# Kernel tuning notes

Measured on AMD Instinct MI355X. Metric: run time of the kernel, lower is better.

Reference implementation:

```python
import jax, jax.numpy as jnp
import numpy as np

N_GROUPS = 32
EPS = 1e-5
N_HEADS = 8
D_K = 64


def setup_inputs() -> dict:
    key = jax.random.key(0)
    ks = jax.random.split(key, 4)
    B, C, H, W = 16, 512, 32, 32
    x = jax.random.normal(ks[0], (B, C, H, W), dtype=jnp.float32)
    gn_w = jnp.ones((C,), dtype=jnp.float32)
    gn_b = jnp.zeros((C,), dtype=jnp.float32)
    proj_w = jax.random.normal(ks[1], (3 * C, C), dtype=jnp.float32) * (C ** -0.5)
    proj_b = jnp.zeros((3 * C,), dtype=jnp.float32)
    out_w = jax.random.normal(ks[2], (C, C), dtype=jnp.float32) * (C ** -0.5)
    out_b = jnp.zeros((C,), dtype=jnp.float32)
    return {"x": x, "gn_w": gn_w, "gn_b": gn_b, "proj_w": proj_w,
            "proj_b": proj_b, "out_w": out_w, "out_b": out_b}


def _group_norm(x, w, b):
    B, C, H, W = x.shape
    xg = x.reshape(B, N_GROUPS, C // N_GROUPS, H, W)
    mean = xg.mean(axis=(2, 3, 4), keepdims=True)
    var = xg.var(axis=(2, 3, 4), keepdims=True)
    xn = (xg - mean) * jax.lax.rsqrt(var + EPS)
    xn = xn.reshape(B, C, H, W)
    return xn * w[None, :, None, None] + b[None, :, None, None]


def reference(x, gn_w, gn_b, proj_w, proj_b, out_w, out_b):
    B, C, H, W = x.shape
    S = H * W
    scale = D_K ** -0.25  # applied to both q and k, as in the original
    h = _group_norm(x, gn_w, gn_b).reshape(B, C, S).transpose(0, 2, 1)  # [B,S,C]
    qkv = h @ proj_w.T + proj_b  # [B,S,3C]
    qkv = qkv.reshape(B, S, N_HEADS, 3 * D_K)
    q, k, v = jnp.split(qkv, 3, axis=-1)  # each [B,S,H,D]
    attn = jnp.einsum('bihd,bjhd->bijh', q * scale, k * scale)  # [B,S,S,Hd]
    attn = jax.nn.softmax(attn, axis=2)
    res = jnp.einsum('bijh,bjhd->bihd', attn, v).reshape(B, S, N_HEADS * D_K)
    res = res @ out_w.T + out_b  # [B,S,C]
    res = res.transpose(0, 2, 1).reshape(B, C, H, W)
    return res + x
```

## Files before the change

### kernel.cpp

```cpp
#include <hip/hip_runtime.h>
#include <stdint.h>

typedef unsigned short u16;
typedef __attribute__((ext_vector_type(8))) short bf16x8;
typedef __attribute__((ext_vector_type(4))) short bf16x4;
typedef __attribute__((ext_vector_type(4))) float f32x4;
typedef __attribute__((ext_vector_type(4))) unsigned short u16x4;

#define GLD16(gp, lp) __builtin_amdgcn_global_load_lds( \
    (__attribute__((address_space(1))) void*)(void*)(gp), \
    (__attribute__((address_space(3))) void*)(void*)(lp), 16, 0, 0)

__device__ __forceinline__ u16 f2b(float f) {
  union { float f; unsigned u; } v; v.f = f;
  unsigned r = v.u + 0x7FFFu + ((v.u >> 16) & 1u);
  return (u16)(r >> 16);
}

__device__ __forceinline__ float fexp2(float x) {
#if __has_builtin(__builtin_amdgcn_exp2f)
  return __builtin_amdgcn_exp2f(x);
#else
  return exp2f(x);
#endif
}

__global__ __launch_bounds__(256) void cvt_kernel(const float* __restrict__ wq_f,
                                                  const float* __restrict__ wo_f,
                                                  u16* __restrict__ wq,
                                                  u16* __restrict__ wo) {
  int i = blockIdx.x * 256 + threadIdx.x;
  const float* src; u16* dst; int j;
  if (i < 196608) { src = wq_f; dst = wq; j = i; }
  else            { src = wo_f; dst = wo; j = i - 196608; }
  const float4 f = ((const float4*)src)[j];
  u16x4 r; r[0] = f2b(f.x); r[1] = f2b(f.y); r[2] = f2b(f.z); r[3] = f2b(f.w);
  *(u16x4*)(dst + (size_t)j * 4) = r;
}

__global__ __launch_bounds__(256) void gn_kernel(const float* __restrict__ x,
                                                 const float* __restrict__ gw,
                                                 const float* __restrict__ gb,
                                                 u16* __restrict__ h) {
  const int b = blockIdx.x >> 5, g = blockIdx.x & 31;
  const float* xg = x + ((size_t)(b * 512 + g * 16)) * 1024;
  const int tid = threadIdx.x;
  float4 vals[16];
  float s = 0.f, ss = 0.f;
#pragma unroll
  for (int j = 0; j < 16; j++) {
    const float4 v = ((const float4*)xg)[j * 256 + tid];
    vals[j] = v;
    s  += (v.x + v.y) + (v.z + v.w);
    ss += (v.x * v.x + v.y * v.y) + (v.z * v.z + v.w * v.w);
  }
#pragma unroll
  for (int off = 32; off; off >>= 1) { s += __shfl_down(s, off); ss += __shfl_down(ss, off); }
  __shared__ float red[8];
  const int wid = tid >> 6, lane = tid & 63;
  if (lane == 0) { red[wid] = s; red[4 + wid] = ss; }
  __syncthreads();
  if (tid == 0) {
    float S = red[0] + red[1] + red[2] + red[3];
    float SS = red[4] + red[5] + red[6] + red[7];
    float mean = S * (1.f / 16384.f);
    float var = SS * (1.f / 16384.f) - mean * mean;
    red[0] = mean; red[1] = rsqrtf(var + 1e-5f);
  }
  __syncthreads();
  const float mean = red[0], rs = red[1];
  float sc[16], bi[16];
#pragma unroll
  for (int c = 0; c < 16; c++) { sc[c] = gw[g * 16 + c] * rs; bi[c] = gb[g * 16 + c]; }
  u16* dst = h + ((size_t)(b * 32 + g) * 1024 + 4 * tid) * 16;
#pragma unroll
  for (int e = 0; e < 4; e++) {
    u16 row[16];
#pragma unroll
    for (int j = 0; j < 16; j++) {
      const float v = (e == 0) ? vals[j].x : (e == 1) ? vals[j].y : (e == 2) ? vals[j].z : vals[j].w;
      row[j] = f2b((v - mean) * sc[j] + bi[j]);
    }
    *(bf16x8*)(dst + e * 16) = *(bf16x8*)&row[0];
    *(bf16x8*)(dst + e * 16 + 8) = *(bf16x8*)&row[8];
  }
}

__global__ __launch_bounds__(256) void qkv_gemm(const u16* __restrict__ h,
                                                const u16* __restrict__ w,
                                                const float* __restrict__ bias,
                                                u16* __restrict__ q,
                                                u16* __restrict__ k,
                                                u16* __restrict__ v) {
  __shared__ u16 As[128 * 32];
  __shared__ u16 Bs[128 * 32];
  const int b = blockIdx.z;
  const int bm = blockIdx.x;
  const int bn = blockIdx.y;
  const int tid = threadIdx.x, lane = tid & 63, wid = tid >> 6;
  const int wm = wid & 1, wn = wid >> 1;
  const u16* gA = h + (size_t)b * 524288 + (size_t)bm * 128 * 16;
  const u16* gB = w + (size_t)bn * 128 * 512;

  const f32x4 fz = {0.f, 0.f, 0.f, 0.f};
  f32x4 acc[4][4];
#pragma unroll
  for (int i = 0; i < 4; i++)
#pragma unroll
    for (int j = 0; j < 4; j++) acc[i][j] = fz;

  const int r0 = lane >> 2;
  const int ch8 = (lane & 3) * 8;

  for (int kt = 0; kt < 16; ++kt) {
    __syncthreads();
    const int chA = kt * 32 + ch8;
    const int gstrip = chA >> 4, rem = chA & 15;
#pragma unroll
    for (int j = 0; j < 2; ++j) {
      const int idx = wid * 2 + j;
      const int row = idx * 16 + r0;
      GLD16(gA + (size_t)gstrip * 16384 + (size_t)row * 16 + rem, &As[idx * 512 + lane * 8]);
      GLD16(gB + (size_t)row * 512 + kt * 32 + ch8, &Bs[idx * 512 + lane * 8]);
    }
    __syncthreads();
    bf16x8 af[4], bf[4];
#pragma unroll
    for (int mi = 0; mi < 4; mi++)
      af[mi] = *(const bf16x8*)&As[(wm * 64 + mi * 16 + (lane & 15)) * 32 + (lane >> 4) * 8];
#pragma unroll
    for (int ni = 0; ni < 4; ni++)
      bf[ni] = *(const bf16x8*)&Bs[(wn * 64 + ni * 16 + (lane & 15)) * 32 + (lane >> 4) * 8];
#pragma unroll
    for (int mi = 0; mi < 4; mi++)
#pragma unroll
      for (int ni = 0; ni < 4; ni++)
        acc[mi][ni] = __builtin_amdgcn_mfma_f32_16x16x32_bf16(af[mi], bf[ni], acc[mi][ni], 0, 0, 0);
  }

  const float qscale = 0.51006972f;
  const float kscale = 0.35355339059327373f;
  const int quad4 = (lane >> 4) << 2;
#pragma unroll
  for (int mi = 0; mi < 4; mi++) {
    const int m = bm * 128 + wm * 64 + mi * 16 + quad4;
#pragma unroll
    for (int ni = 0; ni < 4; ni++) {
      const int n = bn * 128 + wn * 64 + ni * 16 + (lane & 15);
      const int head = n / 192;
      const int rr = n - head * 192;
      const float bi = bias[n];
      const int d = rr & 63;
      if (rr < 128) {
        u16* dst = (rr < 64) ? q : k;
        const float sc = (rr < 64) ? qscale : kscale;
        dst += ((size_t)(b * 8 + head) * 1024 + m) * 64 + d;
#pragma unroll
        for (int r = 0; r < 4; r++)
          dst[(size_t)r * 64] = f2b((acc[mi][ni][r] + bi) * sc);
      } else {
        u16x4 pk;
#pragma unroll
        for (int r = 0; r < 4; r++) pk[r] = f2b(acc[mi][ni][r] + bi);
        *(u16x4*)(v + ((size_t)(b * 8 + head) * 64 + d) * 1024 + m) = pk;
      }
    }
  }
}

__global__ __launch_bounds__(512) void attn_kernel(const u16* __restrict__ q,
                                                   const u16* __restrict__ k,
                                                   const u16* __restrict__ vT,
                                                   u16* __restrict__ o) {
  __shared__ u16 Ks[2][64 * 64];
  __shared__ u16 Vs[2][64 * 64];
  const int bh = blockIdx.x;
  const int qb = blockIdx.y;
  const int tid = threadIdx.x, lane = tid & 63, wid = tid >> 6;
  const u16* Q = q + (size_t)bh * 1024 * 64;
  const u16* K = k + (size_t)bh * 1024 * 64;
  const u16* V = vT + (size_t)bh * 64 * 1024;
  const int qrow0 = qb * 256 + wid * 32;
  const int c15 = lane & 15, quad = lane >> 4;
  const int sw = c15 & 7;
  const int srow = tid >> 3;
  const int u8g  = tid & 7;
  const int s7 = srow & 7;
  const int kld = srow * 64 + ((u8g ^ s7) * 8);
  const int ve = 4 * (u8g >> 2) + 2 * (u8g & 1);
  const int vc = ((u8g >> 1) & 1) * 4;
  const int vld0 = srow * 64 + ((ve ^ s7) * 8) + vc;
  const int vld1 = srow * 64 + (((ve + 1) ^ s7) * 8) + vc;

  bf16x8 qf[2][2];
#pragma unroll
  for (int kk = 0; kk < 2; kk++)
#pragma unroll
    for (int ni = 0; ni < 2; ni++)
      qf[kk][ni] = *(const bf16x8*)(Q + (size_t)(qrow0 + ni * 16 + c15) * 64 + kk * 32 + quad * 8);

  const f32x4 fz = {0.f, 0.f, 0.f, 0.f};
  const float Mshift = 14.4269504089f;
  const f32x4 fm = {-Mshift, -Mshift, -Mshift, -Mshift};
  f32x4 oaccT[4][2];
#pragma unroll
  for (int i = 0; i < 4; i++)
#pragma unroll
    for (int j = 0; j < 2; j++) oaccT[i][j] = fz;
  float lsum[2] = {0.f, 0.f};

  bf16x8 kr, vr;
  kr = *(const bf16x8*)(K + (size_t)srow * 64 + u8g * 8);
  vr = *(const bf16x8*)(V + (size_t)srow * 1024 + u8g * 8);
  {
    u16* Kd = Ks[0]; u16* Vd = Vs[0];
    *(bf16x8*)&Kd[kld] = kr;
    union { bf16x4 h[2]; bf16x8 v; } a; a.v = vr;
    *(bf16x4*)&Vd[vld0] = a.h[0];
    *(bf16x4*)&Vd[vld1] = a.h[1];
  }
  kr = *(const bf16x8*)(K + (size_t)(64 + srow) * 64 + u8g * 8);
  vr = *(const bf16x8*)(V + (size_t)srow * 1024 + 64 + u8g * 8);

  for (int kt = 0; kt < 16; ++kt) {
    __syncthreads();
    const int cur = kt & 1, alt = cur ^ 1;
    if (kt < 15) {
      u16* Kd = Ks[alt]; u16* Vd = Vs[alt];
      *(bf16x8*)&Kd[kld] = kr;
      union { bf16x4 h[2]; bf16x8 v; } a; a.v = vr;
      *(bf16x4*)&Vd[vld0] = a.h[0];
      *(bf16x4*)&Vd[vld1] = a.h[1];
      const int pk2 = (kt + 2) & 15;
      kr = *(const bf16x8*)(K + ((size_t)pk2 * 64 + srow) * 64 + u8g * 8);
      vr = *(const bf16x8*)(V + (size_t)srow * 1024 + pk2 * 64 + u8g * 8);
    }
    const u16* Kc = Ks[cur];
    const u16* Vc = Vs[cur];

    f32x4 sacc[4][2];
#pragma unroll
    for (int i = 0; i < 4; i++)
#pragma unroll
      for (int j = 0; j < 2; j++) sacc[i][j] = fm;
#pragma unroll
    for (int kk = 0; kk < 2; kk++) {
      bf16x8 af[4];
#pragma unroll
      for (int mi = 0; mi < 4; mi++)
        af[mi] = *(const bf16x8*)&Kc[(mi * 16 + c15) * 64 + (((kk * 4 + quad) ^ sw) * 8)];
      __builtin_amdgcn_s_setprio(1);
#pragma unroll
      for (int mi = 0; mi < 4; mi++)
#pragma unroll
        for (int ni = 0; ni < 2; ni++)
          sacc[mi][ni] = __builtin_amdgcn_mfma_f32_16x16x32_bf16(af[mi], qf[kk][ni], sacc[mi][ni], 0, 0, 0);
      __builtin_amdgcn_s_setprio(0);
    }

    unsigned pkd[4][2][2];
#pragma unroll
    for (int ni = 0; ni < 2; ni++) {
      float ls = 0.f;
#pragma unroll
      for (int mi = 0; mi < 4; mi++) {
        unsigned pu[4];
#pragma unroll
        for (int r = 0; r < 4; r++) {
          const float p = fexp2(sacc[mi][ni][r]);
          ls += p;
          union { float f; unsigned u; } c; c.f = p;
          pu[r] = c.u;
        }
        pkd[mi][ni][0] = __builtin_amdgcn_perm(pu[1], pu[0], 0x07060302u);
        pkd[mi][ni][1] = __builtin_amdgcn_perm(pu[3], pu[2], 0x07060302u);
      }
      lsum[ni] += ls;
    }

#pragma unroll
    for (int mg = 0; mg < 2; mg++) {
      union { unsigned u[4]; bf16x8 v; } bb[2];
#pragma unroll
      for (int ni = 0; ni < 2; ni++) {
        bb[ni].u[0] = pkd[2 * mg][ni][0];     bb[ni].u[1] = pkd[2 * mg][ni][1];
        bb[ni].u[2] = pkd[2 * mg + 1][ni][0]; bb[ni].u[3] = pkd[2 * mg + 1][ni][1];
      }
      bf16x8 aa[4];
#pragma unroll
      for (int nd = 0; nd < 4; nd++)
        aa[nd] = *(const bf16x8*)&Vc[(nd * 16 + c15) * 64 + (((mg * 4 + quad) ^ sw) * 8)];
      __builtin_amdgcn_s_setprio(1);
#pragma unroll
      for (int nd = 0; nd < 4; nd++)
#pragma unroll
        for (int ni = 0; ni < 2; ni++)
          oaccT[nd][ni] = __builtin_amdgcn_mfma_f32_16x16x32_bf16(aa[nd], bb[ni].v, oaccT[nd][ni], 0, 0, 0);
      __builtin_amdgcn_s_setprio(0);
    }
  }

  float iv[2];
#pragma unroll
  for (int ni = 0; ni < 2; ni++) {
    float l = lsum[ni];
    l += __shfl_xor(l, 16);
    l += __shfl_xor(l, 32);
    iv[ni] = 1.f / l;
  }
  const int b = bh >> 3, hh = bh & 7;
#pragma unroll
  for (int ni = 0; ni < 2; ni++) {
    const int row = qrow0 + ni * 16 + c15;
#pragma unroll
    for (int nd = 0; nd < 4; nd++) {
      u16x4 pk4;
#pragma unroll
      for (int r = 0; r < 4; r++) pk4[r] = f2b(oaccT[nd][ni][r] * iv[ni]);
      *(u16x4*)(o + ((size_t)b * 1024 + row) * 512 + hh * 64 + nd * 16 + quad * 4) = pk4;
    }
  }
}

__global__ __launch_bounds__(256) void out_gemm(const u16* __restrict__ attn,
                                                const u16* __restrict__ wo,
                                                const float* __restrict__ ob,
                                                const float* __restrict__ x,
                                                float* __restrict__ out) {
  __shared__ u16 As[128 * 32];
  __shared__ u16 Bs[128 * 32];
  const int b = blockIdx.z;
  const int bm = blockIdx.x;
  const int bn = blockIdx.y;
  const int tid = threadIdx.x, lane = tid & 63, wid = tid >> 6;
  const int wm = wid & 1, wn = wid >> 1;
  const u16* gA = attn + ((size_t)b * 1024 + bm * 128) * 512;
  const u16* gB = wo + (size_t)bn * 128 * 512;

  const f32x4 fz = {0.f, 0.f, 0.f, 0.f};
  f32x4 acc[4][4];
#pragma unroll
  for (int i = 0; i < 4; i++)
#pragma unroll
    for (int j = 0; j < 4; j++) acc[i][j] = fz;

  const int r0 = lane >> 2;
  const int ch8 = (lane & 3) * 8;

  for (int kt = 0; kt < 16; ++kt) {
    __syncthreads();
#pragma unroll
    for (int j = 0; j < 2; ++j) {
      const int idx = wid * 2 + j;
      const int row = idx * 16 + r0;
      GLD16(gA + (size_t)row * 512 + kt * 32 + ch8, &As[idx * 512 + lane * 8]);
      GLD16(gB + (size_t)row * 512 + kt * 32 + ch8, &Bs[idx * 512 + lane * 8]);
    }
    __syncthreads();
    bf16x8 af[4], bf[4];
#pragma unroll
    for (int mi = 0; mi < 4; mi++)
      af[mi] = *(const bf16x8*)&As[(wm * 64 + mi * 16 + (lane & 15)) * 32 + (lane >> 4) * 8];
#pragma unroll
    for (int ni = 0; ni < 4; ni++)
      bf[ni] = *(const bf16x8*)&Bs[(wn * 64 + ni * 16 + (lane & 15)) * 32 + (lane >> 4) * 8];
#pragma unroll
    for (int mi = 0; mi < 4; mi++)
#pragma unroll
      for (int ni = 0; ni < 4; ni++)
        acc[mi][ni] = __builtin_amdgcn_mfma_f32_16x16x32_bf16(af[mi], bf[ni], acc[mi][ni], 0, 0, 0);
  }

  const int quad4 = (lane >> 4) << 2;
  const int c15_ = lane & 15;
#pragma unroll
  for (int mi = 0; mi < 4; mi++) {
    const int m = bm * 128 + wm * 64 + mi * 16 + quad4;
#pragma unroll
    for (int ni = 0; ni < 4; ni++) {
      const int c = bn * 128 + wn * 64 + ni * 16 + c15_;
      const float bo = ob[c];
      const size_t idx = ((size_t)b * 512 + c) * 1024 + m;
      const float4 xv = *(const float4*)(x + idx);
      float4 ov;
      ov.x = acc[mi][ni][0] + bo + xv.x;
      ov.y = acc[mi][ni][1] + bo + xv.y;
      ov.z = acc[mi][ni][2] + bo + xv.z;
      ov.w = acc[mi][ni][3] + bo + xv.w;
      *(float4*)(out + idx) = ov;
    }
  }
}

extern "C" void kernel_launch(void* const* d_in, const int* in_sizes, int n_in,
                              void* d_out, int out_size, void* d_ws, size_t ws_size,
                              hipStream_t stream) {
  const float* x      = (const float*)d_in[0];
  const float* gn_w   = (const float*)d_in[1];
  const float* gn_b   = (const float*)d_in[2];
  const float* proj_w = (const float*)d_in[3];
  const float* proj_b = (const float*)d_in[4];
  const float* out_w  = (const float*)d_in[5];
  const float* out_b  = (const float*)d_in[6];
  float* out = (float*)d_out;

  char* p = (char*)d_ws;
  u16* h    = (u16*)p; p += (size_t)16 * 1024 * 512 * 2;
  u16* q    = (u16*)p; p += (size_t)16 * 8 * 1024 * 64 * 2;
  u16* k    = (u16*)p; p += (size_t)16 * 8 * 1024 * 64 * 2;
  u16* v    = (u16*)p; p += (size_t)16 * 8 * 1024 * 64 * 2;
  u16* attn = (u16*)p; p += (size_t)16 * 1024 * 512 * 2;
  u16* wq   = (u16*)p; p += (size_t)1536 * 512 * 2;
  u16* wo   = (u16*)p; p += (size_t)512 * 512 * 2;

  cvt_kernel<<<1024, 256, 0, stream>>>(proj_w, out_w, wq, wo);
  gn_kernel<<<512, 256, 0, stream>>>(x, gn_w, gn_b, h);
  qkv_gemm<<<dim3(8, 12, 16), 256, 0, stream>>>(h, wq, proj_b, q, k, v);
  attn_kernel<<<dim3(128, 4), 512, 0, stream>>>(q, k, v, attn);
  out_gemm<<<dim3(8, 4, 16), 256, 0, stream>>>(attn, wo, out_b, x, out);
}
```

Measured before the change: 210.4 us.

## Merge groupnorm and weight conversion; rewrite QKV GEMM with larger double-buffered tiles

```diff
diff --git a/kernel.cpp b/kernel.cpp
--- a/kernel.cpp
+++ b/kernel.cpp
@@ -25,23 +25,24 @@
 #endif
 }
 
-__global__ __launch_bounds__(256) void cvt_kernel(const float* __restrict__ wq_f,
-                                                  const float* __restrict__ wo_f,
-                                                  u16* __restrict__ wq,
-                                                  u16* __restrict__ wo) {
-  int i = blockIdx.x * 256 + threadIdx.x;
-  const float* src; u16* dst; int j;
-  if (i < 196608) { src = wq_f; dst = wq; j = i; }
-  else            { src = wo_f; dst = wo; j = i - 196608; }
-  const float4 f = ((const float4*)src)[j];
-  u16x4 r; r[0] = f2b(f.x); r[1] = f2b(f.y); r[2] = f2b(f.z); r[3] = f2b(f.w);
-  *(u16x4*)(dst + (size_t)j * 4) = r;
-}
-
-__global__ __launch_bounds__(256) void gn_kernel(const float* __restrict__ x,
-                                                 const float* __restrict__ gw,
-                                                 const float* __restrict__ gb,
-                                                 u16* __restrict__ h) {
+__global__ __launch_bounds__(256) void gncvt_kernel(const float* __restrict__ x,
+                                                    const float* __restrict__ gw,
+                                                    const float* __restrict__ gb,
+                                                    u16* __restrict__ h,
+                                                    const float* __restrict__ wq_f,
+                                                    const float* __restrict__ wo_f,
+                                                    u16* __restrict__ wq,
+                                                    u16* __restrict__ wo) {
+  if (blockIdx.x >= 512) {
+    int i = (blockIdx.x - 512) * 256 + threadIdx.x;
+    const float* src; u16* dst; int j;
+    if (i < 196608) { src = wq_f; dst = wq; j = i; }
+    else            { src = wo_f; dst = wo; j = i - 196608; }
+    const float4 f = ((const float4*)src)[j];
+    u16x4 r; r[0] = f2b(f.x); r[1] = f2b(f.y); r[2] = f2b(f.z); r[3] = f2b(f.w);
+    *(u16x4*)(dst + (size_t)j * 4) = r;
+    return;
+  }
   const int b = blockIdx.x >> 5, g = blockIdx.x & 31;
   const float* xg = x + ((size_t)(b * 512 + g * 16)) * 1024;
   const int tid = threadIdx.x;
@@ -86,67 +87,97 @@
   }
 }
 
-__global__ __launch_bounds__(256) void qkv_gemm(const u16* __restrict__ h,
-                                                const u16* __restrict__ w,
-                                                const float* __restrict__ bias,
-                                                u16* __restrict__ q,
-                                                u16* __restrict__ k,
-                                                u16* __restrict__ v) {
-  __shared__ u16 As[128 * 32];
-  __shared__ u16 Bs[128 * 32];
-  const int b = blockIdx.z;
+__global__ __launch_bounds__(512, 2) void qkv_gemm(const u16* __restrict__ h,
+                                                   const u16* __restrict__ w,
+                                                   const float* __restrict__ bias,
+                                                   u16* __restrict__ q,
+                                                   u16* __restrict__ k,
+                                                   u16* __restrict__ v) {
+  __shared__ u16 As[2][256 * 64];
+  __shared__ u16 Bs[2][256 * 64];
   const int bm = blockIdx.x;
   const int bn = blockIdx.y;
   const int tid = threadIdx.x, lane = tid & 63, wid = tid >> 6;
   const int wm = wid & 1, wn = wid >> 1;
-  const u16* gA = h + (size_t)b * 524288 + (size_t)bm * 128 * 16;
-  const u16* gB = w + (size_t)bn * 128 * 512;
+  const int c15 = lane & 15, quad = lane >> 4;
+  const int sw = c15 & 7;
+  const int b = bm >> 2;
+  const int sp0 = (bm & 3) * 256;
+
+  const int t8 = tid >> 3;
+  const int lc = (tid & 7) ^ (t8 & 7);
+  const u16* pA = h + (size_t)b * 524288 + (size_t)(lc >> 1) * 16384
+                + (size_t)(sp0 + t8) * 16 + (lc & 1) * 8;
+  const u16* pB = w + (size_t)(bn * 256 + t8) * 512 + lc * 8;
 
   const f32x4 fz = {0.f, 0.f, 0.f, 0.f};
-  f32x4 acc[4][4];
-#pragma unroll
-  for (int i = 0; i < 4; i++)
+  f32x4 acc[8][4];
+#pragma unroll
+  for (int i = 0; i < 8; i++)
 #pragma unroll
     for (int j = 0; j < 4; j++) acc[i][j] = fz;
 
-  const int r0 = lane >> 2;
-  const int ch8 = (lane & 3) * 8;
-
-  for (int kt = 0; kt < 16; ++kt) {
-    __syncthreads();
-    const int chA = kt * 32 + ch8;
-    const int gstrip = chA >> 4, rem = chA & 15;
-#pragma unroll
-    for (int j = 0; j < 2; ++j) {
-      const int idx = wid * 2 + j;
-      const int row = idx * 16 + r0;
-      GLD16(gA + (size_t)gstrip * 16384 + (size_t)row * 16 + rem, &As[idx * 512 + lane * 8]);
-      GLD16(gB + (size_t)row * 512 + kt * 32 + ch8, &Bs[idx * 512 + lane * 8]);
-    }
-    __syncthreads();
-    bf16x8 af[4], bf[4];
-#pragma unroll
-    for (int mi = 0; mi < 4; mi++)
-      af[mi] = *(const bf16x8*)&As[(wm * 64 + mi * 16 + (lane & 15)) * 32 + (lane >> 4) * 8];
-#pragma unroll
-    for (int ni = 0; ni < 4; ni++)
-      bf[ni] = *(const bf16x8*)&Bs[(wn * 64 + ni * 16 + (lane & 15)) * 32 + (lane >> 4) * 8];
-#pragma unroll
-    for (int mi = 0; mi < 4; mi++)
+#pragma unroll
+  for (int i = 0; i < 4; i++) {
+    GLD16(pA + (size_t)i * 1024, &As[0][(i * 512 + tid) * 8]);
+    GLD16(pB + (size_t)i * 32768, &Bs[0][(i * 512 + tid) * 8]);
+  }
+  asm volatile("s_waitcnt vmcnt(0)" ::: "memory");
+  __builtin_amdgcn_s_barrier();
+  __builtin_amdgcn_sched_barrier(0);
+
+  for (int kt = 0; kt < 8; ++kt) {
+    const int cb = kt & 1, db = cb ^ 1;
+    if (kt < 7) {
+#pragma unroll
+      for (int i = 0; i < 4; i++) {
+        GLD16(pA + (size_t)(kt + 1) * 65536 + (size_t)i * 1024, &As[db][(i * 512 + tid) * 8]);
+        GLD16(pB + (size_t)(kt + 1) * 64 + (size_t)i * 32768, &Bs[db][(i * 512 + tid) * 8]);
+      }
+      __builtin_amdgcn_sched_barrier(0);
+    }
+    bf16x8 bfx[2][4];
+#pragma unroll
+    for (int kk = 0; kk < 2; kk++) {
+      const int kc = ((kk * 4 + quad) ^ sw) * 8;
 #pragma unroll
       for (int ni = 0; ni < 4; ni++)
-        acc[mi][ni] = __builtin_amdgcn_mfma_f32_16x16x32_bf16(af[mi], bf[ni], acc[mi][ni], 0, 0, 0);
+        bfx[kk][ni] = *(const bf16x8*)&Bs[cb][(wn * 64 + ni * 16 + c15) * 64 + kc];
+    }
+#pragma unroll
+    for (int ph = 0; ph < 2; ph++) {
+      bf16x8 af[2][4];
+#pragma unroll
+      for (int kk = 0; kk < 2; kk++) {
+        const int kc = ((kk * 4 + quad) ^ sw) * 8;
+#pragma unroll
+        for (int mi = 0; mi < 4; mi++)
+          af[kk][mi] = *(const bf16x8*)&As[cb][(wm * 128 + ph * 64 + mi * 16 + c15) * 64 + kc];
+      }
+      __builtin_amdgcn_s_setprio(1);
+#pragma unroll
+      for (int kk = 0; kk < 2; kk++)
+#pragma unroll
+        for (int mi = 0; mi < 4; mi++)
+#pragma unroll
+          for (int ni = 0; ni < 4; ni++)
+            acc[ph * 4 + mi][ni] = __builtin_amdgcn_mfma_f32_16x16x32_bf16(af[kk][mi], bfx[kk][ni], acc[ph * 4 + mi][ni], 0, 0, 0);
+      __builtin_amdgcn_s_setprio(0);
+    }
+    asm volatile("s_waitcnt vmcnt(0)" ::: "memory");
+    __builtin_amdgcn_s_barrier();
+    __builtin_amdgcn_sched_barrier(0);
   }
 
   const float qscale = 0.51006972f;
   const float kscale = 0.35355339059327373f;
-  const int quad4 = (lane >> 4) << 2;
-#pragma unroll
-  for (int mi = 0; mi < 4; mi++) {
-    const int m = bm * 128 + wm * 64 + mi * 16 + quad4;
+  const int quad4 = quad << 2;
+#pragma unroll
+  for (int mi = 0; mi < 8; mi++) {
+    const int sp = sp0 + wm * 128 + mi * 16 + quad4;
 #pragma unroll
     for (int ni = 0; ni < 4; ni++) {
-      const int n = bn * 128 + wn * 64 + ni * 16 + (lane & 15);
+      const int n = bn * 256 + wn * 64 + ni * 16 + c15;
       const int head = n / 192;
       const int rr = n - head * 192;
       const float bi = bias[n];
@@ -154,7 +185,7 @@
       if (rr < 128) {
         u16* dst = (rr < 64) ? q : k;
         const float sc = (rr < 64) ? qscale : kscale;
-        dst += ((size_t)(b * 8 + head) * 1024 + m) * 64 + d;
+        dst += ((size_t)(b * 8 + head) * 1024 + sp) * 64 + d;
 #pragma unroll
         for (int r = 0; r < 4; r++)
           dst[(size_t)r * 64] = f2b((acc[mi][ni][r] + bi) * sc);
@@ -162,7 +193,7 @@
         u16x4 pk;
 #pragma unroll
         for (int r = 0; r < 4; r++) pk[r] = f2b(acc[mi][ni][r] + bi);
-        *(u16x4*)(v + ((size_t)(b * 8 + head) * 64 + d) * 1024 + m) = pk;
+        *(u16x4*)(v + ((size_t)(b * 8 + head) * 64 + d) * 1024 + sp) = pk;
       }
     }
   }
@@ -413,9 +444,8 @@
   u16* wq   = (u16*)p; p += (size_t)1536 * 512 * 2;
   u16* wo   = (u16*)p; p += (size_t)512 * 512 * 2;
 
-  cvt_kernel<<<1024, 256, 0, stream>>>(proj_w, out_w, wq, wo);
-  gn_kernel<<<512, 256, 0, stream>>>(x, gn_w, gn_b, h);
-  qkv_gemm<<<dim3(8, 12, 16), 256, 0, stream>>>(h, wq, proj_b, q, k, v);
+  gncvt_kernel<<<1536, 256, 0, stream>>>(x, gn_w, gn_b, h, proj_w, out_w, wq, wo);
+  qkv_gemm<<<dim3(64, 6), 512, 0, stream>>>(h, wq, proj_b, q, k, v);
   attn_kernel<<<dim3(128, 4), 512, 0, stream>>>(q, k, v, attn);
   out_gemm<<<dim3(8, 4, 16), 256, 0, stream>>>(attn, wo, out_b, x, out);
 }
```

Result: faster. 204.1 us (-3.0%).
